# Optimization experiments

Measured on AMD Instinct MI355X. Metric: run time of the kernel, lower is better.

The kernel has to match this reference:

```python
import jax, jax.numpy as jnp
import numpy as np
from jax import lax

K = 7            # cfg.network.PSROI_BINS == pool_size
FEAT_STRIDE = 16
LAMDA = 0.1
D_PER_BIN = 8    # feature channels per position-sensitive bin -> C = K*K*8 = 392


def _bilinear(feat, y, x, extra_idx):
    """Bilinearly sample feat[H,W,...] at float coords (y,x); extra_idx are
    integer index arrays (broadcast to y.shape) selecting trailing feat axes."""
    H, W = feat.shape[0], feat.shape[1]
    y0f = jnp.floor(y); x0f = jnp.floor(x)
    wy = (y - y0f)[..., None]
    wx = (x - x0f)[..., None]
    y0 = jnp.clip(y0f.astype(jnp.int32), 0, H - 1)
    y1 = jnp.clip(y0f.astype(jnp.int32) + 1, 0, H - 1)
    x0 = jnp.clip(x0f.astype(jnp.int32), 0, W - 1)
    x1 = jnp.clip(x0f.astype(jnp.int32) + 1, 0, W - 1)
    def g(yi, xi):
        return feat[(yi, xi) + extra_idx]
    return ((1 - wy) * (1 - wx) * g(y0, x0) + (1 - wy) * wx * g(y0, x1)
            + wy * (1 - wx) * g(y1, x0) + wy * wx * g(y1, x1))


def ps_roi(f, rois, k, feat_stride, offsets=None):
    """Position-sensitive RoI pooling. f: [H,W,C] with C = k*k*D (bin-major
    channel layout). rois: [N,5] (batch, x1, y1, x2, y2) in image coords.
    offsets (optional): [N, k*k, G, 2] per-bin, per-channel-group (x,y) shifts
    in image coords. Returns [N, D, k, k]."""
    H, W, C = f.shape
    N = rois.shape[0]
    kk = k * k
    D = C // kk
    x1 = rois[:, 1] / feat_stride
    y1 = rois[:, 2] / feat_stride
    x2 = (rois[:, 3] + 1.0) / feat_stride
    y2 = (rois[:, 4] + 1.0) / feat_stride
    bw = (x2 - x1) / k  # [N]
    bh = (y2 - y1) / k
    jj = jnp.tile(jnp.arange(k, dtype=f.dtype), k)     # bin = i*k + j
    ii = jnp.repeat(jnp.arange(k, dtype=f.dtype), k)
    cx = x1[:, None] + (jj + 0.5) * bw[:, None]        # [N, kk] bin centers
    cy = y1[:, None] + (ii + 0.5) * bh[:, None]
    bins = jnp.arange(kk, dtype=jnp.int32)
    if offsets is None:
        feat = f.reshape(H, W, kk, D)
        b = jnp.broadcast_to(bins, (N, kk))
        vals = _bilinear(feat, cy, cx, (b,))           # [N, kk, D]
    else:
        G = offsets.shape[2]
        cxg = cx[:, :, None] + offsets[..., 0] / feat_stride  # [N, kk, G]
        cyg = cy[:, :, None] + offsets[..., 1] / feat_stride
        feat = f.reshape(H, W, kk, G, D // G)
        b = jnp.broadcast_to(bins[None, :, None], (N, kk, G))
        g = jnp.broadcast_to(jnp.arange(G, dtype=jnp.int32)[None, None, :], (N, kk, G))
        vals = _bilinear(feat, cyg, cxg, (b, g))       # [N, kk, G, D//G]
        vals = vals.reshape(N, kk, D)
    return jnp.transpose(vals.reshape(N, k, k, D), (0, 3, 1, 2))  # [N, D, k, k]


def setup_inputs():
    key = jax.random.key(0)
    kf, kw, k1, k2 = jax.random.split(key, 4)
    H = W = 128
    C = K * K * D_PER_BIN
    N = 2048
    features = jax.random.normal(kf, (1, H, W, C), jnp.float32)
    conv_w = jax.random.normal(kw, (3, 3, C, 2 * 4 * K * K), jnp.float32) * 0.01
    img = float(H * FEAT_STRIDE)
    xy1 = jax.random.uniform(k1, (N, 2), minval=0.0, maxval=img * 0.6)
    wh = jax.random.uniform(k2, (N, 2), minval=32.0, maxval=img * 0.4)
    xy2 = jnp.minimum(xy1 + wh, img - 1.0)
    rois = jnp.concatenate([jnp.zeros((N, 1)), xy1[:, :1], xy1[:, 1:], xy2[:, :1], xy2[:, 1:]], axis=1).astype(jnp.float32)
    return {"features": features, "rois": rois, "conv_w": conv_w}


def reference(features, rois, conv_w):
    # offset branch: 3x3 conv (no bias) -> PS-RoI pool -> scale by lamda*roi size
    offset_map = lax.conv_general_dilated(features, conv_w, (1, 1), 'SAME',
                                          dimension_numbers=('NHWC', 'HWIO', 'NHWC'))
    off = ps_roi(offset_map[0], rois, K, FEAT_STRIDE)          # [N, 8, K, K]
    N = off.shape[0]
    off = off.reshape(N, -1, 2, K, K)                          # [N, 4, 2, K, K]
    off = jnp.transpose(off, (2, 3, 4, 1, 0))                  # [2, K, K, 4, N]
    roi_w = rois[:, 3] - rois[:, 1] + 1.0
    roi_h = rois[:, 4] - rois[:, 2] + 1.0
    off = jnp.stack((off[0] * roi_w * LAMDA, off[1] * roi_h * LAMDA), axis=0)
    off = jnp.transpose(off, (4, 1, 2, 3, 0))                  # [N, K, K, 4, 2]
    off = off.reshape(N, K * K, -1, 2)                         # [N, kk, 4, 2]
    # deformable PS-RoI pooling of the features with predicted offsets
    return ps_roi(features[0], rois, K, FEAT_STRIDE, offsets=off)  # [N, 8, K, K]
```

## Files before the change

### kernel.cpp

```cpp
#include <hip/hip_runtime.h>
#include <hip/hip_cooperative_groups.h>
#include <cstddef>
#include <cstdint>

namespace cg = cooperative_groups;

#define HH    128
#define WW    128
#define CC    392
#define NPIX  (HH*WW)
#define NROI  2048
#define PSK   7
#define NBIN  49
#define LAMDA 0.1f

#define CPAD      448
#define HPAD      130
#define NPADCO    416
#define SEGSTRIDE (9*CPAD)
#define BKK       64
#define NQ        63

#define NBLK    1024
#define NTHR    256
#define GSTRIDE (NBLK*NTHR)
#define FTOT    (HPAD*HPAD*(CPAD/8))
#define WTILES  (9*14*13)
#define POOL8   (NROI*NBIN*8)

typedef _Float16 half8   __attribute__((ext_vector_type(8)));
typedef _Float16 half2v  __attribute__((ext_vector_type(2)));
typedef float    floatx4 __attribute__((ext_vector_type(4)));

__device__ __forceinline__ void async_ld16(const _Float16* g, _Float16* l) {
  __builtin_amdgcn_global_load_lds((const __attribute__((address_space(1))) void*)g,
                                   (__attribute__((address_space(3))) void*)l,
                                   16, 0, 0);
}

__device__ __forceinline__ void prep_features(const float* __restrict__ F,
                                              _Float16* __restrict__ Fh,
                                              int gtid, int stride) {
  for (int idx = gtid; idx < FTOT; idx += stride) {
    const int p   = idx / (CPAD / 8);
    const int cgi = idx - p * (CPAD / 8);
    const int c   = cgi * 8;
    const int py  = p / HPAD;
    const int px  = p - py * HPAD;
    half8 h;
#pragma unroll
    for (int i = 0; i < 8; ++i) h[i] = (_Float16)0.f;
    if (py >= 1 && py <= HH && px >= 1 && px <= WW && c < CC) {
      const float* src = F + ((size_t)(py - 1) * WW + (px - 1)) * CC + c;
      const float4 v0 = *(const float4*)src;
      const float4 v1 = *(const float4*)(src + 4);
      h[0] = (_Float16)v0.x; h[1] = (_Float16)v0.y;
      h[2] = (_Float16)v0.z; h[3] = (_Float16)v0.w;
      h[4] = (_Float16)v1.x; h[5] = (_Float16)v1.y;
      h[6] = (_Float16)v1.z; h[7] = (_Float16)v1.w;
    }
    *(half8*)(Fh + (size_t)p * CPAD + c) = h;
  }
}

__device__ __forceinline__ void prep_weights(const float* __restrict__ Wt,
                                             _Float16* __restrict__ Bth,
                                             float (*tile)[33],
                                             int bid, int t, int nblocks) {
  for (int tl = bid; tl < WTILES; tl += nblocks) {
    const int seg = tl / (14 * 13);
    const int rem = tl - seg * (14 * 13);
    const int cit = rem / 13;
    const int cot = rem - cit * 13;
    const int ci0 = cit * 32, co0 = cot * 32;
    __syncthreads();
#pragma unroll
    for (int i = 0; i < 4; ++i) {
      const int idx = t + i * 256;
      const int lr = idx >> 5;
      const int lc = idx & 31;
      const int ci = ci0 + lr, co = co0 + lc;
      float v = 0.f;
      if (ci < CC && co < CC) v = Wt[((size_t)seg * CC + ci) * CC + co];
      tile[lr][lc] = v;
    }
    __syncthreads();
#pragma unroll
    for (int i = 0; i < 4; ++i) {
      const int idx = t + i * 256;
      const int lr = idx >> 5;
      const int lc = idx & 31;
      Bth[(size_t)(co0 + lr) * SEGSTRIDE + seg * CPAD + ci0 + lc] = (_Float16)tile[lc][lr];
    }
  }
}

__device__ __forceinline__ void conv_fat(const _Float16* __restrict__ Fh,
                                         const _Float16* __restrict__ Bth,
                                         _Float16* __restrict__ OMp,
                                         _Float16* As, _Float16* Bs,
                                         int row0, int col0, int q0, int q1, int t) {
  const int L = t & 63;
  const int w = t >> 6;

  const int srow = L >> 3;
  const int kofs = ((L & 7) ^ srow) * 8;
  const int ya = row0 >> 7;
  const int nbase = col0 + w * 32 + srow;

  const int wm = (w >> 1) * 64;
  const int wn = (w & 1) * 64;
  const int fr = L & 15;
  const int quad = L >> 4;
  const int pg0 = (quad ^ (fr & 7)) * 8;
  const int pg1 = ((4 + quad) ^ (fr & 7)) * 8;

  floatx4 acc[4][4];
#pragma unroll
  for (int i = 0; i < 4; ++i)
#pragma unroll
    for (int j = 0; j < 4; ++j) {
      floatx4 z = {0.f, 0.f, 0.f, 0.f};
      acc[i][j] = z;
    }

  for (int q = q0; q < q1; ++q) {
    const int seg = q / 7;
    const int it  = q - seg * 7;
    const int dy = seg / 3 - 1;
    const int dx = seg - (seg / 3) * 3 - 1;
    const int fy = ya + 1 + dy;
    const int cb = it * BKK;
    const _Float16* gArow = Fh + ((size_t)fy * HPAD + (1 + dx)) * CPAD + kofs + cb;
    const _Float16* gB = Bth + (size_t)nbase * SEGSTRIDE + seg * CPAD + kofs + cb;

#pragma unroll
    for (int j = 0; j < 4; ++j) {
      const int xr = w * 32 + j * 8 + srow;
      async_ld16(gArow + (size_t)xr * CPAD, &As[(w * 32 + j * 8) * BKK]);
    }
#pragma unroll
    for (int j = 0; j < 4; ++j)
      async_ld16(gB + (size_t)(j * 8) * SEGSTRIDE, &Bs[(w * 32 + j * 8) * BKK]);
    __syncthreads();

    half8 a0[4], a1[4], b0[4], b1[4];
#pragma unroll
    for (int mt = 0; mt < 4; ++mt) {
      const int rb = (wm + mt * 16 + fr) * BKK;
      a0[mt] = *(const half8*)(&As[rb + pg0]);
      a1[mt] = *(const half8*)(&As[rb + pg1]);
    }
#pragma unroll
    for (int nt = 0; nt < 4; ++nt) {
      const int rb = (wn + nt * 16 + fr) * BKK;
      b0[nt] = *(const half8*)(&Bs[rb + pg0]);
      b1[nt] = *(const half8*)(&Bs[rb + pg1]);
    }
#pragma unroll
    for (int mt = 0; mt < 4; ++mt)
#pragma unroll
      for (int nt = 0; nt < 4; ++nt)
        acc[mt][nt] = __builtin_amdgcn_mfma_f32_16x16x32_f16(a0[mt], b0[nt], acc[mt][nt], 0, 0, 0);
#pragma unroll
    for (int mt = 0; mt < 4; ++mt)
#pragma unroll
      for (int nt = 0; nt < 4; ++nt)
        acc[mt][nt] = __builtin_amdgcn_mfma_f32_16x16x32_f16(a1[mt], b1[nt], acc[mt][nt], 0, 0, 0);
    __syncthreads();
  }

#pragma unroll
  for (int mt = 0; mt < 4; ++mt) {
    const int rbase = row0 + wm + mt * 16 + quad * 4;
#pragma unroll
    for (int nt = 0; nt < 4; ++nt) {
      const int col = col0 + wn + nt * 16 + fr;
      if (col < CC) {
#pragma unroll
        for (int r = 0; r < 4; ++r)
          OMp[(size_t)(rbase + r) * CC + col] = (_Float16)acc[mt][nt][r];
      }
    }
  }
}

__device__ __forceinline__ void conv_thin(const _Float16* __restrict__ Fh,
                                          const _Float16* __restrict__ Bth,
                                          _Float16* __restrict__ OMp,
                                          _Float16* As, _Float16* Bs,
                                          int row0, int q0, int q1, int t) {
  const int L = t & 63;
  const int w = t >> 6;

  const int srow = L >> 3;
  const int kofs = ((L & 7) ^ srow) * 8;
  const int ya = row0 >> 7;
  const int nbase = 384 + w * 8 + srow;

  const int wm = w * 32;
  const int fr = L & 15;
  const int quad = L >> 4;
  const int pg0 = (quad ^ (fr & 7)) * 8;
  const int pg1 = ((4 + quad) ^ (fr & 7)) * 8;

  floatx4 acc[2];
#pragma unroll
  for (int i = 0; i < 2; ++i) {
    floatx4 z = {0.f, 0.f, 0.f, 0.f};
    acc[i] = z;
  }

  for (int q = q0; q < q1; ++q) {
    const int seg = q / 7;
    const int it  = q - seg * 7;
    const int dy = seg / 3 - 1;
    const int dx = seg - (seg / 3) * 3 - 1;
    const int fy = ya + 1 + dy;
    const int cb = it * BKK;
    const _Float16* gArow = Fh + ((size_t)fy * HPAD + (1 + dx)) * CPAD + kofs + cb;

#pragma unroll
    for (int j = 0; j < 4; ++j) {
      const int xr = w * 32 + j * 8 + srow;
      async_ld16(gArow + (size_t)xr * CPAD, &As[(w * 32 + j * 8) * BKK]);
    }
    if (w < 2) {
      const _Float16* gB = Bth + (size_t)nbase * SEGSTRIDE + seg * CPAD + kofs + cb;
      async_ld16(gB, &Bs[(w * 8) * BKK]);
    }
    __syncthreads();

    half8 a0[2], a1[2];
#pragma unroll
    for (int mt = 0; mt < 2; ++mt) {
      const int rb = (wm + mt * 16 + fr) * BKK;
      a0[mt] = *(const half8*)(&As[rb + pg0]);
      a1[mt] = *(const half8*)(&As[rb + pg1]);
    }
    const half8 b0 = *(const half8*)(&Bs[fr * BKK + pg0]);
    const half8 b1 = *(const half8*)(&Bs[fr * BKK + pg1]);
#pragma unroll
    for (int mt = 0; mt < 2; ++mt)
      acc[mt] = __builtin_amdgcn_mfma_f32_16x16x32_f16(a0[mt], b0, acc[mt], 0, 0, 0);
#pragma unroll
    for (int mt = 0; mt < 2; ++mt)
      acc[mt] = __builtin_amdgcn_mfma_f32_16x16x32_f16(a1[mt], b1, acc[mt], 0, 0, 0);
    __syncthreads();
  }

#pragma unroll
  for (int mt = 0; mt < 2; ++mt) {
    const int rbase = row0 + wm + mt * 16 + quad * 4;
    const int col = 384 + fr;
    if (col < CC) {
#pragma unroll
      for (int r = 0; r < 4; ++r)
        OMp[(size_t)(rbase + r) * CC + col] = (_Float16)acc[mt][r];
    }
  }
}

__device__ __forceinline__ void conv_dispatch(const _Float16* Fh, const _Float16* Bth,
                                              _Float16* OMa, _Float16* OMb,
                                              _Float16* As, _Float16* Bs,
                                              int bid, int t) {
  const int x = bid & 127;
  const int rest = bid >> 7;
  const int kz = (rest < 6) ? (rest / 3) : (rest - 6);
  _Float16* OMp = kz ? OMb : OMa;
  const int q0 = kz * 32;
  const int q1 = kz ? NQ : 32;
  if (rest < 6)
    conv_fat(Fh, Bth, OMp, As, Bs, x * 128, (rest % 3) * 128, q0, q1, t);
  else
    conv_thin(Fh, Bth, OMp, As, Bs, x * 128, q0, q1, t);
}

__device__ __forceinline__ void bilin_setup(float y, float x,
                                            int& iy0, int& iy1, int& ix0, int& ix1,
                                            float& w00, float& w01, float& w10, float& w11) {
  const float y0f = floorf(y), x0f = floorf(x);
  const float wy = y - y0f, wx = x - x0f;
  const int a = (int)y0f, b = (int)x0f;
  iy0 = min(max(a, 0), HH - 1);
  iy1 = min(max(a + 1, 0), HH - 1);
  ix0 = min(max(b, 0), WW - 1);
  ix1 = min(max(b + 1, 0), WW - 1);
  w00 = (1.f - wy) * (1.f - wx);
  w01 = (1.f - wy) * wx;
  w10 = wy * (1.f - wx);
  w11 = wy * wx;
}

__device__ __forceinline__ void pool_item8(const _Float16* __restrict__ Fh,
                                           const float* __restrict__ R,
                                           const _Float16* __restrict__ OMa,
                                           const _Float16* __restrict__ OMb,
                                           float* __restrict__ out, int tid) {
  const int j  = tid & 7;
  const int nb = tid >> 3;
  const int n  = nb / NBIN;
  const int b  = nb - n * NBIN;
  const int bi = b / PSK;
  const int bj = b - bi * PSK;

  const float rx1 = R[n * 5 + 1], ry1 = R[n * 5 + 2];
  const float rx2 = R[n * 5 + 3], ry2 = R[n * 5 + 4];
  const float x1 = rx1 * (1.f / 16.f);
  const float y1 = ry1 * (1.f / 16.f);
  const float x2 = (rx2 + 1.f) * (1.f / 16.f);
  const float y2 = (ry2 + 1.f) * (1.f / 16.f);
  const float bw = (x2 - x1) * (1.f / 7.f);
  const float bh = (y2 - y1) * (1.f / 7.f);
  const float cx = x1 + ((float)bj + 0.5f) * bw;
  const float cy = y1 + ((float)bi + 0.5f) * bh;
  const float sxs = (rx2 - rx1 + 1.f) * (LAMDA / 16.f);
  const float sys = (ry2 - ry1 + 1.f) * (LAMDA / 16.f);

  int iy0, iy1, ix0, ix1;
  float w00, w01, w10, w11;
  bilin_setup(cy, cx, iy0, iy1, ix0, ix1, w00, w01, w10, w11);

  const int c = j & 3;
  const int cyi = (c >> 1) ? iy1 : iy0;
  const int cxi = (c & 1) ? ix1 : ix0;
  const float wq = (c == 0) ? w00 : (c == 1) ? w01 : (c == 2) ? w10 : w11;

  const _Float16* OMp = (j >> 2) ? OMb : OMa;
  const size_t base = (size_t)(cyi * WW + cxi) * CC + (size_t)b * 8;
  const half8 hv = *(const half8*)(OMp + base);

  float o8[8];
#pragma unroll
  for (int i = 0; i < 8; ++i) o8[i] = wq * (float)hv[i];
#pragma unroll
  for (int i = 0; i < 8; ++i) o8[i] += __shfl_xor(o8[i], 1);
#pragma unroll
  for (int i = 0; i < 8; ++i) o8[i] += __shfl_xor(o8[i], 2);
#pragma unroll
  for (int i = 0; i < 8; ++i) o8[i] += __shfl_xor(o8[i], 4);

  const int g = j & 3;
  const float sx = cx + o8[2 * g] * sxs;
  const float sy = cy + o8[2 * g + 1] * sys;

  int jy0, jy1, jx0, jx1;
  float u00, u01, u10, u11;
  bilin_setup(sy, sx, jy0, jy1, jx0, jx1, u00, u01, u10, u11);

  const int  yh = j >> 2;
  const int  jy = yh ? jy1 : jy0;
  const float ua = yh ? u10 : u00;
  const float ub = yh ? u11 : u01;

  const size_t c0 = (size_t)b * 8 + 2 * g;
  const half2v qa = *(const half2v*)(Fh + ((size_t)(jy + 1) * HPAD + (jx0 + 1)) * CPAD + c0);
  const half2v qb = *(const half2v*)(Fh + ((size_t)(jy + 1) * HPAD + (jx1 + 1)) * CPAD + c0);

  float v0 = ua * (float)qa[0] + ub * (float)qb[0];
  float v1 = ua * (float)qa[1] + ub * (float)qb[1];
  v0 += __shfl_xor(v0, 4);
  v1 += __shfl_xor(v1, 4);

  const float vout = yh ? v1 : v0;
  out[((size_t)n * 8 + 2 * g + yh) * NBIN + b] = vout;
}

__global__ __launch_bounds__(NTHR, 4)
void mega_kernel(const float* __restrict__ F, const float* __restrict__ Wt,
                 _Float16* __restrict__ OMa, _Float16* __restrict__ OMb,
                 _Float16* __restrict__ Fh, _Float16* __restrict__ Bth) {
  __shared__ __align__(16) _Float16 smem[2 * 128 * BKK];
  const int bid = blockIdx.x;
  const int t = threadIdx.x;
  cg::grid_group grid = cg::this_grid();

  prep_features(F, Fh, bid * NTHR + t, GSTRIDE);
  prep_weights(Wt, Bth, (float(*)[33])smem, bid, t, NBLK);

  __threadfence();
  grid.sync();

  conv_dispatch(Fh, Bth, OMa, OMb, smem, smem + 128 * BKK, bid, t);
}

__global__ __launch_bounds__(256)
void pool_kernel(const _Float16* __restrict__ Fh, const float* __restrict__ R,
                 const _Float16* __restrict__ OMa, const _Float16* __restrict__ OMb,
                 float* __restrict__ out) {
  pool_item8(Fh, R, OMa, OMb, out, blockIdx.x * 256 + threadIdx.x);
}

__global__ __launch_bounds__(256)
void prep_kernel_sa(const float* __restrict__ F, const float* __restrict__ Wt,
                    _Float16* __restrict__ Fh, _Float16* __restrict__ Bth) {
  __shared__ float tile[32][33];
  prep_features(F, Fh, blockIdx.x * 256 + threadIdx.x, gridDim.x * 256);
  prep_weights(Wt, Bth, tile, blockIdx.x, threadIdx.x, gridDim.x);
}

__global__ __launch_bounds__(256, 4)
void conv_kernel_sa(const _Float16* __restrict__ Fh, const _Float16* __restrict__ Bth,
                    _Float16* __restrict__ OMa, _Float16* __restrict__ OMb) {
  __shared__ __align__(16) _Float16 smem[2 * 128 * BKK];
  conv_dispatch(Fh, Bth, OMa, OMb, smem, smem + 128 * BKK, blockIdx.x, threadIdx.x);
}

extern "C" void kernel_launch(void* const* d_in, const int* in_sizes, int n_in,
                              void* d_out, int out_size, void* d_ws, size_t ws_size,
                              hipStream_t stream) {
  const float* F  = (const float*)d_in[0];
  const float* R  = (const float*)d_in[1];
  const float* Wt = (const float*)d_in[2];
  float* out = (float*)d_out;

  const size_t omBytes  = (size_t)NPIX * CC * sizeof(_Float16);
  const size_t fhBytes  = (size_t)HPAD * HPAD * CPAD * sizeof(_Float16);

  _Float16* OMa = (_Float16*)d_ws;
  _Float16* OMb = OMa + (size_t)NPIX * CC;
  _Float16* Fh  = (_Float16*)((char*)d_ws + 2 * omBytes);
  _Float16* Bth = (_Float16*)((char*)d_ws + 2 * omBytes + fhBytes);

  int maxBlk = 0;
  hipError_t qerr = hipOccupancyMaxActiveBlocksPerMultiprocessor(&maxBlk, mega_kernel, NTHR, 0);
  bool coopOk = (qerr == hipSuccess && maxBlk >= 4);

  if (coopOk) {
    void* args[] = {(void*)&F, (void*)&Wt, (void*)&OMa, (void*)&OMb,
                    (void*)&Fh, (void*)&Bth};
    hipError_t err = hipLaunchCooperativeKernel((const void*)mega_kernel,
                                                dim3(NBLK), dim3(NTHR),
                                                args, 0, stream);
    if (err != hipSuccess) {
      (void)hipGetLastError();
      coopOk = false;
    }
  }
  if (!coopOk) {
    prep_kernel_sa<<<2048, 256, 0, stream>>>(F, Wt, Fh, Bth);
    conv_kernel_sa<<<NBLK, 256, 0, stream>>>(Fh, Bth, OMa, OMb);
  }

  pool_kernel<<<POOL8 / 256, 256, 0, stream>>>(Fh, R, OMa, OMb, out);
}
```

Measured before the change: 157.4 us.

## Double-buffer conv K-tiles with 32-wide chunks and prefetch next stage

The conv GEMM main loop changes from a single 64-wide K tile with load, sync and compute per step to a double-buffered pipeline over 32-wide K chunks. Each step issues async global-to-LDS loads for the next chunk, then runs MFMAs on the current one. A lighter barrier (waitcnt plus s_barrier) replaces the second __syncthreads. The aim is to hide global load latency behind MFMA work, at the cost of twice as many loop iterations, half the MFMAs per step, and dropping the XOR LDS swizzle, which may add bank conflicts.

New measurement: 174.7 us. 1.11x slower.

```diff
diff --git a/kernel.cpp b/kernel.cpp
--- a/kernel.cpp
+++ b/kernel.cpp
@@ -18,8 +18,10 @@
 #define HPAD      130
 #define NPADCO    416
 #define SEGSTRIDE (9*CPAD)
-#define BKK       64
-#define NQ        63
+#define BKC       32
+#define NQT       126
+#define QSPLIT    63
+#define TH        (128*BKC)
 
 #define NBLK    1024
 #define NTHR    256
@@ -95,25 +97,67 @@
   }
 }
 
+__device__ __forceinline__ void stage_a(const _Float16* __restrict__ Fh,
+                                        int ya, int q, _Float16* Ab, int t) {
+  const int L = t & 63, w = t >> 6;
+  const int seg = q / 14;
+  const int it  = q - seg * 14;
+  const int dy = seg / 3 - 1;
+  const int dx = seg - (seg / 3) * 3 - 1;
+  const int fy = ya + 1 + dy;
+  const int cb = it * BKC + (L & 3) * 8;
+  const int rl = L >> 2;
+  const _Float16* gA = Fh + ((size_t)fy * HPAD + (1 + dx)) * CPAD + cb;
+#pragma unroll
+  for (int j = 0; j < 2; ++j)
+    async_ld16(gA + (size_t)(w * 32 + j * 16 + rl) * CPAD,
+               Ab + (w * 32 + j * 16) * BKC);
+}
+
+__device__ __forceinline__ void stage_b_fat(const _Float16* __restrict__ Bth,
+                                            int col0, int q, _Float16* Bb, int t) {
+  const int L = t & 63, w = t >> 6;
+  const int seg = q / 14;
+  const int it  = q - seg * 14;
+  const int cb = it * BKC + (L & 3) * 8;
+  const int rl = L >> 2;
+  const _Float16* gB = Bth + (size_t)(col0 + w * 32 + rl) * SEGSTRIDE + seg * CPAD + cb;
+#pragma unroll
+  for (int j = 0; j < 2; ++j)
+    async_ld16(gB + (size_t)(j * 16) * SEGSTRIDE,
+               Bb + (w * 32 + j * 16) * BKC);
+}
+
+__device__ __forceinline__ void stage_b_thin(const _Float16* __restrict__ Bth,
+                                             int q, _Float16* Bb, int t) {
+  const int L = t & 63, w = t >> 6;
+  if (w != 0) return;
+  const int seg = q / 14;
+  const int it  = q - seg * 14;
+  const int cb = it * BKC + (L & 3) * 8;
+  const int rl = L >> 2;
+  const _Float16* gB = Bth + (size_t)(384 + rl) * SEGSTRIDE + seg * CPAD + cb;
+  async_ld16(gB, Bb);
+}
+
+__device__ __forceinline__ void step_sync() {
+  asm volatile("s_waitcnt vmcnt(0)" ::: "memory");
+  __builtin_amdgcn_s_barrier();
+  asm volatile("" ::: "memory");
+}
+
 __device__ __forceinline__ void conv_fat(const _Float16* __restrict__ Fh,
                                          const _Float16* __restrict__ Bth,
                                          _Float16* __restrict__ OMp,
-                                         _Float16* As, _Float16* Bs,
+                                         _Float16* __restrict__ smem,
                                          int row0, int col0, int q0, int q1, int t) {
   const int L = t & 63;
   const int w = t >> 6;
-
-  const int srow = L >> 3;
-  const int kofs = ((L & 7) ^ srow) * 8;
   const int ya = row0 >> 7;
-  const int nbase = col0 + w * 32 + srow;
-
+  const int fr = L & 15;
+  const int quad = L >> 4;
   const int wm = (w >> 1) * 64;
   const int wn = (w & 1) * 64;
-  const int fr = L & 15;
-  const int quad = L >> 4;
-  const int pg0 = (quad ^ (fr & 7)) * 8;
-  const int pg1 = ((4 + quad) ^ (fr & 7)) * 8;
 
   floatx4 acc[4][4];
 #pragma unroll
@@ -124,50 +168,33 @@
       acc[i][j] = z;
     }
 
+  stage_a(Fh, ya, q0, smem, t);
+  stage_b_fat(Bth, col0, q0, smem + TH, t);
+  step_sync();
+
+  int off = 0;
   for (int q = q0; q < q1; ++q) {
-    const int seg = q / 7;
-    const int it  = q - seg * 7;
-    const int dy = seg / 3 - 1;
-    const int dx = seg - (seg / 3) * 3 - 1;
-    const int fy = ya + 1 + dy;
-    const int cb = it * BKK;
-    const _Float16* gArow = Fh + ((size_t)fy * HPAD + (1 + dx)) * CPAD + kofs + cb;
-    const _Float16* gB = Bth + (size_t)nbase * SEGSTRIDE + seg * CPAD + kofs + cb;
-
-#pragma unroll
-    for (int j = 0; j < 4; ++j) {
-      const int xr = w * 32 + j * 8 + srow;
-      async_ld16(gArow + (size_t)xr * CPAD, &As[(w * 32 + j * 8) * BKK]);
-    }
-#pragma unroll
-    for (int j = 0; j < 4; ++j)
-      async_ld16(gB + (size_t)(j * 8) * SEGSTRIDE, &Bs[(w * 32 + j * 8) * BKK]);
-    __syncthreads();
-
-    half8 a0[4], a1[4], b0[4], b1[4];
-#pragma unroll
-    for (int mt = 0; mt < 4; ++mt) {
-      const int rb = (wm + mt * 16 + fr) * BKK;
-      a0[mt] = *(const half8*)(&As[rb + pg0]);
-      a1[mt] = *(const half8*)(&As[rb + pg1]);
-    }
-#pragma unroll
-    for (int nt = 0; nt < 4; ++nt) {
-      const int rb = (wn + nt * 16 + fr) * BKK;
-      b0[nt] = *(const half8*)(&Bs[rb + pg0]);
-      b1[nt] = *(const half8*)(&Bs[rb + pg1]);
-    }
+    const int noff = off ^ (2 * TH);
+    if (q + 1 < q1) {
+      stage_a(Fh, ya, q + 1, smem + noff, t);
+      stage_b_fat(Bth, col0, q + 1, smem + noff + TH, t);
+    }
+    const _Float16* Ab = smem + off;
+    const _Float16* Bb = smem + off + TH;
+    half8 a[4], b[4];
 #pragma unroll
     for (int mt = 0; mt < 4; ++mt)
+      a[mt] = *(const half8*)(Ab + (size_t)(wm + mt * 16 + fr) * BKC + quad * 8);
+#pragma unroll
+    for (int nt = 0; nt < 4; ++nt)
+      b[nt] = *(const half8*)(Bb + (size_t)(wn + nt * 16 + fr) * BKC + quad * 8);
+#pragma unroll
+    for (int mt = 0; mt < 4; ++mt)
 #pragma unroll
       for (int nt = 0; nt < 4; ++nt)
-        acc[mt][nt] = __builtin_amdgcn_mfma_f32_16x16x32_f16(a0[mt], b0[nt], acc[mt][nt], 0, 0, 0);
-#pragma unroll
-    for (int mt = 0; mt < 4; ++mt)
-#pragma unroll
-      for (int nt = 0; nt < 4; ++nt)
-        acc[mt][nt] = __builtin_amdgcn_mfma_f32_16x16x32_f16(a1[mt], b1[nt], acc[mt][nt], 0, 0, 0);
-    __syncthreads();
+        acc[mt][nt] = __builtin_amdgcn_mfma_f32_16x16x32_f16(a[mt], b[nt], acc[mt][nt], 0, 0, 0);
+    step_sync();
+    off = noff;
   }
 
 #pragma unroll
@@ -188,21 +215,14 @@
 __device__ __forceinline__ void conv_thin(const _Float16* __restrict__ Fh,
                                           const _Float16* __restrict__ Bth,
                                           _Float16* __restrict__ OMp,
-                                          _Float16* As, _Float16* Bs,
+                                          _Float16* __restrict__ smem,
                                           int row0, int q0, int q1, int t) {
   const int L = t & 63;
   const int w = t >> 6;
-
-  const int srow = L >> 3;
-  const int kofs = ((L & 7) ^ srow) * 8;
   const int ya = row0 >> 7;
-  const int nbase = 384 + w * 8 + srow;
-
-  const int wm = w * 32;
   const int fr = L & 15;
   const int quad = L >> 4;
-  const int pg0 = (quad ^ (fr & 7)) * 8;
-  const int pg1 = ((4 + quad) ^ (fr & 7)) * 8;
+  const int wm = w * 32;
 
   floatx4 acc[2];
 #pragma unroll
@@ -211,42 +231,29 @@
     acc[i] = z;
   }
 
+  stage_a(Fh, ya, q0, smem, t);
+  stage_b_thin(Bth, q0, smem + TH, t);
+  step_sync();
+
+  int off = 0;
   for (int q = q0; q < q1; ++q) {
-    const int seg = q / 7;
-    const int it  = q - seg * 7;
-    const int dy = seg / 3 - 1;
-    const int dx = seg - (seg / 3) * 3 - 1;
-    const int fy = ya + 1 + dy;
-    const int cb = it * BKK;
-    const _Float16* gArow = Fh + ((size_t)fy * HPAD + (1 + dx)) * CPAD + kofs + cb;
-
-#pragma unroll
-    for (int j = 0; j < 4; ++j) {
-      const int xr = w * 32 + j * 8 + srow;
-      async_ld16(gArow + (size_t)xr * CPAD, &As[(w * 32 + j * 8) * BKK]);
-    }
-    if (w < 2) {
-      const _Float16* gB = Bth + (size_t)nbase * SEGSTRIDE + seg * CPAD + kofs + cb;
-      async_ld16(gB, &Bs[(w * 8) * BKK]);
-    }
-    __syncthreads();
-
-    half8 a0[2], a1[2];
-#pragma unroll
-    for (int mt = 0; mt < 2; ++mt) {
-      const int rb = (wm + mt * 16 + fr) * BKK;
-      a0[mt] = *(const half8*)(&As[rb + pg0]);
-      a1[mt] = *(const half8*)(&As[rb + pg1]);
-    }
-    const half8 b0 = *(const half8*)(&Bs[fr * BKK + pg0]);
-    const half8 b1 = *(const half8*)(&Bs[fr * BKK + pg1]);
+    const int noff = off ^ (2 * TH);
+    if (q + 1 < q1) {
+      stage_a(Fh, ya, q + 1, smem + noff, t);
+      stage_b_thin(Bth, q + 1, smem + noff + TH, t);
+    }
+    const _Float16* Ab = smem + off;
+    const _Float16* Bb = smem + off + TH;
+    half8 a[2];
 #pragma unroll
     for (int mt = 0; mt < 2; ++mt)
-      acc[mt] = __builtin_amdgcn_mfma_f32_16x16x32_f16(a0[mt], b0, acc[mt], 0, 0, 0);
+      a[mt] = *(const half8*)(Ab + (size_t)(wm + mt * 16 + fr) * BKC + quad * 8);
+    const half8 b = *(const half8*)(Bb + (size_t)fr * BKC + quad * 8);
 #pragma unroll
     for (int mt = 0; mt < 2; ++mt)
-      acc[mt] = __builtin_amdgcn_mfma_f32_16x16x32_f16(a1[mt], b1, acc[mt], 0, 0, 0);
-    __syncthreads();
+      acc[mt] = __builtin_amdgcn_mfma_f32_16x16x32_f16(a[mt], b, acc[mt], 0, 0, 0);
+    step_sync();
+    off = noff;
   }
 
 #pragma unroll
@@ -263,18 +270,17 @@
 
 __device__ __forceinline__ void conv_dispatch(const _Float16* Fh, const _Float16* Bth,
                                               _Float16* OMa, _Float16* OMb,
-                                              _Float16* As, _Float16* Bs,
-                                              int bid, int t) {
+                                              _Float16* smem, int bid, int t) {
   const int x = bid & 127;
   const int rest = bid >> 7;
   const int kz = (rest < 6) ? (rest / 3) : (rest - 6);
   _Float16* OMp = kz ? OMb : OMa;
-  const int q0 = kz * 32;
-  const int q1 = kz ? NQ : 32;
+  const int q0 = kz * QSPLIT;
+  const int q1 = kz ? NQT : QSPLIT;
   if (rest < 6)
-    conv_fat(Fh, Bth, OMp, As, Bs, x * 128, (rest % 3) * 128, q0, q1, t);
+    conv_fat(Fh, Bth, OMp, smem, x * 128, (rest % 3) * 128, q0, q1, t);
   else
-    conv_thin(Fh, Bth, OMp, As, Bs, x * 128, q0, q1, t);
+    conv_thin(Fh, Bth, OMp, smem, x * 128, q0, q1, t);
 }
 
 __device__ __forceinline__ void bilin_setup(float y, float x,
@@ -371,7 +377,7 @@
 void mega_kernel(const float* __restrict__ F, const float* __restrict__ Wt,
                  _Float16* __restrict__ OMa, _Float16* __restrict__ OMb,
                  _Float16* __restrict__ Fh, _Float16* __restrict__ Bth) {
-  __shared__ __align__(16) _Float16 smem[2 * 128 * BKK];
+  __shared__ __align__(16) _Float16 smem[4 * TH];
   const int bid = blockIdx.x;
   const int t = threadIdx.x;
   cg::grid_group grid = cg::this_grid();
@@ -382,7 +388,7 @@
   __threadfence();
   grid.sync();
 
-  conv_dispatch(Fh, Bth, OMa, OMb, smem, smem + 128 * BKK, bid, t);
+  conv_dispatch(Fh, Bth, OMa, OMb, smem, bid, t);
 }
 
 __global__ __launch_bounds__(256)
@@ -403,8 +409,8 @@
 __global__ __launch_bounds__(256, 4)
 void conv_kernel_sa(const _Float16* __restrict__ Fh, const _Float16* __restrict__ Bth,
                     _Float16* __restrict__ OMa, _Float16* __restrict__ OMb) {
-  __shared__ __align__(16) _Float16 smem[2 * 128 * BKK];
-  conv_dispatch(Fh, Bth, OMa, OMb, smem, smem + 128 * BKK, blockIdx.x, threadIdx.x);
+  __shared__ __align__(16) _Float16 smem[4 * TH];
+  conv_dispatch(Fh, Bth, OMa, OMb, smem, blockIdx.x, threadIdx.x);
 }
 
 extern "C" void kernel_launch(void* const* d_in, const int* in_sizes, int n_in,
```

## Reuse one staged 130-row A tile across the three horizontal conv taps

Applied to the files above, without the earlier changes.

The implicit-GEMM conv now stages a 130-row (padded to 136) strip of the feature row once per (dy, channel-chunk), then reads it at row shifts 0, 1 and 2 for the three dx taps, loading only the B tile per tap. This removes two of every three A-tile global loads. The split-K boundary moves from 32/63 steps to 10/21 row-chunks, which shifts the work balance between the two partial outputs. The cost is slightly larger LDS, an extra sync per tap, and swizzle math that depends on the shifted row.

New measurement: 150.8 us. 1.04x faster.

```diff
diff --git a/kernel.cpp b/kernel.cpp
--- a/kernel.cpp
+++ b/kernel.cpp
@@ -19,7 +19,12 @@
 #define NPADCO    416
 #define SEGSTRIDE (9*CPAD)
 #define BKK       64
-#define NQ        63
+#define NSS       21
+#define SSPLIT    10
+
+#define AROWS   136
+#define ATH     (AROWS*BKK)
+#define BTH     (128*BKK)
 
 #define NBLK    1024
 #define NTHR    256
@@ -95,11 +100,29 @@
   }
 }
 
+__device__ __forceinline__ void stage_a130(const _Float16* __restrict__ Fh,
+                                           int fy, int cb, _Float16* As, int t) {
+  const int L = t & 63, w = t >> 6;
+  const int srow = L >> 3;
+  const int kofs = ((L & 7) ^ srow) * 8;
+  const _Float16* gA = Fh + (size_t)fy * HPAD * CPAD + kofs + cb;
+#pragma unroll
+  for (int j = 0; j < 4; ++j) {
+    const int r = w * 32 + j * 8 + srow;
+    async_ld16(gA + (size_t)r * CPAD, &As[(w * 32 + j * 8) * BKK]);
+  }
+  if (w == 0) {
+    const int r = 128 + srow;
+    const int rp = (r <= 129) ? r : 129;
+    async_ld16(gA + (size_t)rp * CPAD, &As[128 * BKK]);
+  }
+}
+
 __device__ __forceinline__ void conv_fat(const _Float16* __restrict__ Fh,
                                          const _Float16* __restrict__ Bth,
                                          _Float16* __restrict__ OMp,
                                          _Float16* As, _Float16* Bs,
-                                         int row0, int col0, int q0, int q1, int t) {
+                                         int row0, int col0, int s0, int s1, int t) {
   const int L = t & 63;
   const int w = t >> 6;
 
@@ -112,8 +135,6 @@
   const int wn = (w & 1) * 64;
   const int fr = L & 15;
   const int quad = L >> 4;
-  const int pg0 = (quad ^ (fr & 7)) * 8;
-  const int pg1 = ((4 + quad) ^ (fr & 7)) * 8;
 
   floatx4 acc[4][4];
 #pragma unroll
@@ -124,50 +145,49 @@
       acc[i][j] = z;
     }
 
-  for (int q = q0; q < q1; ++q) {
-    const int seg = q / 7;
-    const int it  = q - seg * 7;
-    const int dy = seg / 3 - 1;
-    const int dx = seg - (seg / 3) * 3 - 1;
-    const int fy = ya + 1 + dy;
-    const int cb = it * BKK;
-    const _Float16* gArow = Fh + ((size_t)fy * HPAD + (1 + dx)) * CPAD + kofs + cb;
-    const _Float16* gB = Bth + (size_t)nbase * SEGSTRIDE + seg * CPAD + kofs + cb;
-
-#pragma unroll
-    for (int j = 0; j < 4; ++j) {
-      const int xr = w * 32 + j * 8 + srow;
-      async_ld16(gArow + (size_t)xr * CPAD, &As[(w * 32 + j * 8) * BKK]);
-    }
-#pragma unroll
-    for (int j = 0; j < 4; ++j)
-      async_ld16(gB + (size_t)(j * 8) * SEGSTRIDE, &Bs[(w * 32 + j * 8) * BKK]);
-    __syncthreads();
-
-    half8 a0[4], a1[4], b0[4], b1[4];
-#pragma unroll
-    for (int mt = 0; mt < 4; ++mt) {
-      const int rb = (wm + mt * 16 + fr) * BKK;
-      a0[mt] = *(const half8*)(&As[rb + pg0]);
-      a1[mt] = *(const half8*)(&As[rb + pg1]);
-    }
-#pragma unroll
-    for (int nt = 0; nt < 4; ++nt) {
-      const int rb = (wn + nt * 16 + fr) * BKK;
-      b0[nt] = *(const half8*)(&Bs[rb + pg0]);
-      b1[nt] = *(const half8*)(&Bs[rb + pg1]);
-    }
-#pragma unroll
-    for (int mt = 0; mt < 4; ++mt)
-#pragma unroll
-      for (int nt = 0; nt < 4; ++nt)
-        acc[mt][nt] = __builtin_amdgcn_mfma_f32_16x16x32_f16(a0[mt], b0[nt], acc[mt][nt], 0, 0, 0);
-#pragma unroll
-    for (int mt = 0; mt < 4; ++mt)
-#pragma unroll
-      for (int nt = 0; nt < 4; ++nt)
-        acc[mt][nt] = __builtin_amdgcn_mfma_f32_16x16x32_f16(a1[mt], b1[nt], acc[mt][nt], 0, 0, 0);
-    __syncthreads();
+  for (int s = s0; s < s1; ++s) {
+    const int dyi = s / 7;
+    const int it  = s - dyi * 7;
+    const int fy  = ya + dyi;
+    const int cb  = it * BKK;
+
+    stage_a130(Fh, fy, cb, As, t);
+
+    for (int dxs = 0; dxs < 3; ++dxs) {
+      const int seg = dyi * 3 + dxs;
+      const _Float16* gB = Bth + (size_t)nbase * SEGSTRIDE + seg * CPAD + kofs + cb;
+#pragma unroll
+      for (int j = 0; j < 4; ++j)
+        async_ld16(gB + (size_t)(j * 8) * SEGSTRIDE, &Bs[(w * 32 + j * 8) * BKK]);
+      __syncthreads();
+
+      half8 a0[4], a1[4], b0[4], b1[4];
+#pragma unroll
+      for (int mt = 0; mt < 4; ++mt) {
+        const int row = wm + mt * 16 + fr + dxs;
+        const int rk = row & 7;
+        a0[mt] = *(const half8*)(&As[row * BKK + ((quad ^ rk) * 8)]);
+        a1[mt] = *(const half8*)(&As[row * BKK + (((4 + quad) ^ rk) * 8)]);
+      }
+#pragma unroll
+      for (int nt = 0; nt < 4; ++nt) {
+        const int rb = (wn + nt * 16 + fr) * BKK;
+        const int rk = fr & 7;
+        b0[nt] = *(const half8*)(&Bs[rb + ((quad ^ rk) * 8)]);
+        b1[nt] = *(const half8*)(&Bs[rb + (((4 + quad) ^ rk) * 8)]);
+      }
+#pragma unroll
+      for (int mt = 0; mt < 4; ++mt)
+#pragma unroll
+        for (int nt = 0; nt < 4; ++nt)
+          acc[mt][nt] = __builtin_amdgcn_mfma_f32_16x16x32_f16(a0[mt], b0[nt], acc[mt][nt], 0, 0, 0);
+#pragma unroll
+      for (int mt = 0; mt < 4; ++mt)
+#pragma unroll
+        for (int nt = 0; nt < 4; ++nt)
+          acc[mt][nt] = __builtin_amdgcn_mfma_f32_16x16x32_f16(a1[mt], b1[nt], acc[mt][nt], 0, 0, 0);
+      __syncthreads();
+    }
   }
 
 #pragma unroll
@@ -189,7 +209,7 @@
                                           const _Float16* __restrict__ Bth,
                                           _Float16* __restrict__ OMp,
                                           _Float16* As, _Float16* Bs,
-                                          int row0, int q0, int q1, int t) {
+                                          int row0, int s0, int s1, int t) {
   const int L = t & 63;
   const int w = t >> 6;
 
@@ -201,8 +221,6 @@
   const int wm = w * 32;
   const int fr = L & 15;
   const int quad = L >> 4;
-  const int pg0 = (quad ^ (fr & 7)) * 8;
-  const int pg1 = ((4 + quad) ^ (fr & 7)) * 8;
 
   floatx4 acc[2];
 #pragma unroll
@@ -211,42 +229,41 @@
     acc[i] = z;
   }
 
-  for (int q = q0; q < q1; ++q) {
-    const int seg = q / 7;
-    const int it  = q - seg * 7;
-    const int dy = seg / 3 - 1;
-    const int dx = seg - (seg / 3) * 3 - 1;
-    const int fy = ya + 1 + dy;
-    const int cb = it * BKK;
-    const _Float16* gArow = Fh + ((size_t)fy * HPAD + (1 + dx)) * CPAD + kofs + cb;
-
-#pragma unroll
-    for (int j = 0; j < 4; ++j) {
-      const int xr = w * 32 + j * 8 + srow;
-      async_ld16(gArow + (size_t)xr * CPAD, &As[(w * 32 + j * 8) * BKK]);
-    }
-    if (w < 2) {
-      const _Float16* gB = Bth + (size_t)nbase * SEGSTRIDE + seg * CPAD + kofs + cb;
-      async_ld16(gB, &Bs[(w * 8) * BKK]);
-    }
-    __syncthreads();
-
-    half8 a0[2], a1[2];
-#pragma unroll
-    for (int mt = 0; mt < 2; ++mt) {
-      const int rb = (wm + mt * 16 + fr) * BKK;
-      a0[mt] = *(const half8*)(&As[rb + pg0]);
-      a1[mt] = *(const half8*)(&As[rb + pg1]);
-    }
-    const half8 b0 = *(const half8*)(&Bs[fr * BKK + pg0]);
-    const half8 b1 = *(const half8*)(&Bs[fr * BKK + pg1]);
-#pragma unroll
-    for (int mt = 0; mt < 2; ++mt)
-      acc[mt] = __builtin_amdgcn_mfma_f32_16x16x32_f16(a0[mt], b0, acc[mt], 0, 0, 0);
-#pragma unroll
-    for (int mt = 0; mt < 2; ++mt)
-      acc[mt] = __builtin_amdgcn_mfma_f32_16x16x32_f16(a1[mt], b1, acc[mt], 0, 0, 0);
-    __syncthreads();
+  for (int s = s0; s < s1; ++s) {
+    const int dyi = s / 7;
+    const int it  = s - dyi * 7;
+    const int fy  = ya + dyi;
+    const int cb  = it * BKK;
+
+    stage_a130(Fh, fy, cb, As, t);
+
+    for (int dxs = 0; dxs < 3; ++dxs) {
+      const int seg = dyi * 3 + dxs;
+      if (w < 2) {
+        const _Float16* gB = Bth + (size_t)nbase * SEGSTRIDE + seg * CPAD + kofs + cb;
+        async_ld16(gB, &Bs[(w * 8) * BKK]);
+      }
+      __syncthreads();
+
+      half8 a0[2], a1[2];
+#pragma unroll
+      for (int mt = 0; mt < 2; ++mt) {
+        const int row = wm + mt * 16 + fr + dxs;
+        const int rk = row & 7;
+        a0[mt] = *(const half8*)(&As[row * BKK + ((quad ^ rk) * 8)]);
+        a1[mt] = *(const half8*)(&As[row * BKK + (((4 + quad) ^ rk) * 8)]);
+      }
+      const int rk = fr & 7;
+      const half8 b0 = *(const half8*)(&Bs[fr * BKK + ((quad ^ rk) * 8)]);
+      const half8 b1 = *(const half8*)(&Bs[fr * BKK + (((4 + quad) ^ rk) * 8)]);
+#pragma unroll
+      for (int mt = 0; mt < 2; ++mt)
+        acc[mt] = __builtin_amdgcn_mfma_f32_16x16x32_f16(a0[mt], b0, acc[mt], 0, 0, 0);
+#pragma unroll
+      for (int mt = 0; mt < 2; ++mt)
+        acc[mt] = __builtin_amdgcn_mfma_f32_16x16x32_f16(a1[mt], b1, acc[mt], 0, 0, 0);
+      __syncthreads();
+    }
   }
 
 #pragma unroll
@@ -269,12 +286,12 @@
   const int rest = bid >> 7;
   const int kz = (rest < 6) ? (rest / 3) : (rest - 6);
   _Float16* OMp = kz ? OMb : OMa;
-  const int q0 = kz * 32;
-  const int q1 = kz ? NQ : 32;
+  const int s0 = kz ? SSPLIT : 0;
+  const int s1 = kz ? NSS : SSPLIT;
   if (rest < 6)
-    conv_fat(Fh, Bth, OMp, As, Bs, x * 128, (rest % 3) * 128, q0, q1, t);
+    conv_fat(Fh, Bth, OMp, As, Bs, x * 128, (rest % 3) * 128, s0, s1, t);
   else
-    conv_thin(Fh, Bth, OMp, As, Bs, x * 128, q0, q1, t);
+    conv_thin(Fh, Bth, OMp, As, Bs, x * 128, s0, s1, t);
 }
 
 __device__ __forceinline__ void bilin_setup(float y, float x,
@@ -371,7 +388,7 @@
 void mega_kernel(const float* __restrict__ F, const float* __restrict__ Wt,
                  _Float16* __restrict__ OMa, _Float16* __restrict__ OMb,
                  _Float16* __restrict__ Fh, _Float16* __restrict__ Bth) {
-  __shared__ __align__(16) _Float16 smem[2 * 128 * BKK];
+  __shared__ __align__(16) _Float16 smem[ATH + BTH];
   const int bid = blockIdx.x;
   const int t = threadIdx.x;
   cg::grid_group grid = cg::this_grid();
@@ -382,7 +399,7 @@
   __threadfence();
   grid.sync();
 
-  conv_dispatch(Fh, Bth, OMa, OMb, smem, smem + 128 * BKK, bid, t);
+  conv_dispatch(Fh, Bth, OMa, OMb, smem, smem + ATH, bid, t);
 }
 
 __global__ __launch_bounds__(256)
@@ -403,8 +420,8 @@
 __global__ __launch_bounds__(256, 4)
 void conv_kernel_sa(const _Float16* __restrict__ Fh, const _Float16* __restrict__ Bth,
                     _Float16* __restrict__ OMa, _Float16* __restrict__ OMb) {
-  __shared__ __align__(16) _Float16 smem[2 * 128 * BKK];
-  conv_dispatch(Fh, Bth, OMa, OMb, smem, smem + 128 * BKK, blockIdx.x, threadIdx.x);
+  __shared__ __align__(16) _Float16 smem[ATH + BTH];
+  conv_dispatch(Fh, Bth, OMa, OMb, smem, smem + ATH, blockIdx.x, threadIdx.x);
 }
 
 extern "C" void kernel_launch(void* const* d_in, const int* in_sizes, int n_in,
```
